# Performance work log

Hardware: AMD Instinct MI355X
Metric: run time of the kernel (lower is better)

Reference implementation:

```python
import jax, jax.numpy as jnp
import numpy as np

N_E = 8192
E_DIM = 64
BETA = 0.25
N_TOKENS = 32768


def setup_inputs() -> dict:
    key = jax.random.key(0)
    k1, k2 = jax.random.split(key)
    x = jax.random.normal(k1, (N_TOKENS, E_DIM), dtype=jnp.float32)
    # nn.Embedding weight initialized uniform(-1/n_e, 1/n_e)
    codebook = jax.random.uniform(k2, (N_E, E_DIM), dtype=jnp.float32,
                                  minval=-1.0 / N_E, maxval=1.0 / N_E)
    return {"x": x, "codebook": codebook, "start": 0, "end": N_E, "use_sk": 0}


def reference(x, codebook, start, end, use_sk):
    # use_sk=0 -> argmin branch (sinkhorn branch calls external helper, not exercised)
    latent = x.reshape(-1, E_DIM)                       # [N, D]
    cb = codebook[start:end]                            # [K, D]
    # squared euclidean distances: ||z||^2 + ||e||^2 - 2 z.e
    d = (jnp.sum(latent * latent, axis=1, keepdims=True)
         + jnp.sum(cb * cb, axis=1)[None, :]
         - 2.0 * jnp.einsum('nd,kd->nk', latent, cb))   # [N, K]
    indices = jnp.argmin(d, axis=-1) + start            # [N]
    x_q = codebook[indices].reshape(x.shape)            # gather
    sg = jax.lax.stop_gradient
    commitment_loss = jnp.mean((sg(x_q) - x) ** 2)
    codebook_loss = jnp.mean((x_q - sg(x)) ** 2)
    loss = codebook_loss + BETA * commitment_loss
    x_q_st = x + sg(x_q - x)                            # straight-through estimator
    indices = indices.reshape(x.shape[:-1])
    return x_q_st, loss, indices
```

## Files before the change

### kernel.cpp

```cpp
#include <hip/hip_runtime.h>
#include <math.h>


#define N_E    8192
#define EDIM   64
#define NTOK   32768
#define NELEM  (NTOK * EDIM)
#define CSZ    32
#define WINDOW 3e-4f
#define TTOK   128
#define TCODE  1024
#define SROW   72
#define TOKB   16
#define KCAP   256

typedef __attribute__((ext_vector_type(8)))  short          short8;
typedef __attribute__((ext_vector_type(8)))  unsigned short ushort8v;
typedef __attribute__((ext_vector_type(16))) float          f32x16;

__device__ __forceinline__ unsigned short f2bf(float f) {
  unsigned int u = __float_as_uint(f);
  return (unsigned short)((u + 0x7FFFu + ((u >> 16) & 1u)) >> 16);
}
__device__ __forceinline__ unsigned short f2h(float f) {
  union { _Float16 h; unsigned short u; } cv; cv.h = (_Float16)f; return cv.u;
}
__device__ __forceinline__ float h2f(unsigned short b) {
  union { _Float16 h; unsigned short u; } cv; cv.u = b; return (float)cv.h;
}
__device__ __forceinline__ float max16(const f32x16 a) {
  float m = fmaxf(fmaxf(a[0], a[1]), a[2]);
  m = fmaxf(fmaxf(m, a[3]),  a[4]);
  m = fmaxf(fmaxf(m, a[5]),  a[6]);
  m = fmaxf(fmaxf(m, a[7]),  a[8]);
  m = fmaxf(fmaxf(m, a[9]),  a[10]);
  m = fmaxf(fmaxf(m, a[11]), a[12]);
  m = fmaxf(fmaxf(m, a[13]), a[14]);
  return fmaxf(m, a[15]);
}
__device__ __forceinline__ float sx_of(const float4* xl4) {
#pragma clang fp contract(off)
  float a0=0,a1=0,a2=0,a3=0,a4=0,a5=0,a6=0,a7=0;
#pragma unroll
  for (int i = 0; i < 8; ++i) {
    float4 pA = xl4[2*i], pB = xl4[2*i+1];
    a0 += pA.x * pA.x; a1 += pA.y * pA.y; a2 += pA.z * pA.z; a3 += pA.w * pA.w;
    a4 += pB.x * pB.x; a5 += pB.y * pB.y; a6 += pB.z * pB.z; a7 += pB.w * pB.w;
  }
  return ((a0+a1) + (a2+a3)) + ((a4+a5) + (a6+a7));
}

__global__ __launch_bounds__(256) void vq_sc(const float* __restrict__ cb,
                                             float* __restrict__ sc,
                                             unsigned short* __restrict__ cbf) {
#pragma clang fp contract(off)
  int r = blockIdx.x * 256 + threadIdx.x;
  const float4* c4 = (const float4*)(cb + (size_t)r * EDIM);
  float sval = sx_of(c4);
  sc[r] = sval;
  unsigned short* dst = cbf + (size_t)r * EDIM;
#pragma unroll
  for (int h = 0; h < 8; ++h) {
    float4 fA = c4[2*h], fB = c4[2*h+1];
    ushort8v o = {f2bf(fA.x), f2bf(fA.y), f2bf(fA.z), f2bf(fA.w),
                  f2bf(fB.x), f2bf(fB.y), f2bf(fB.z), f2bf(fB.w)};
    *(ushort8v*)&dst[h * 8] = o;
  }
}

__global__ __launch_bounds__(256, 4) void vq_pass1(
    const float* __restrict__ x, const unsigned short* __restrict__ cbf,
    unsigned int* __restrict__ cand,
    const int* __restrict__ p_start, const int* __restrict__ p_end) {
  __shared__ unsigned short Cs[128 * SROW];
  __shared__ unsigned minL[128 * 17];
  int tid = threadIdx.x;
  int tb = blockIdx.x;
  int cbk = blockIdx.y;
  int s = *p_start, e = *p_end;
  const bool allfull = (cbk * TCODE >= s) && (cbk * TCODE + TCODE <= e);

  int lane = tid & 63, wv = tid >> 6;
  int half = lane >> 5, ln = lane & 31;
  int tokbase = wv * 32;

  const ushort8v* cg0 = (const ushort8v*)(cbf + (size_t)cbk * TCODE * EDIM);
#pragma unroll
  for (int p = 0; p < 4; ++p) {
    int idx = tid + p * 256;
    int row = idx >> 3, h = idx & 7;
    *(ushort8v*)&Cs[row * SROW + h * 8] = cg0[idx];
  }

  short8 bfr[4];
  {
    const float* xrow =
        x + (size_t)(tb * TTOK + tokbase + ln) * EDIM + half * 8;
#pragma unroll
    for (int ks = 0; ks < 4; ++ks) {
      float4 fA = *(const float4*)(xrow + ks * 16);
      float4 fB = *(const float4*)(xrow + ks * 16 + 4);
      short8 v = {(short)f2bf(fA.x), (short)f2bf(fA.y), (short)f2bf(fA.z),
                  (short)f2bf(fA.w), (short)f2bf(fB.x), (short)f2bf(fB.y),
                  (short)f2bf(fB.z), (short)f2bf(fB.w)};
      bfr[ks] = v;
    }
  }
  __syncthreads();

  unsigned short* minL16 = (unsigned short*)minL;

  for (int nb = 0; nb < 8; ++nb) {
    ushort8v creg[4];
    if (nb < 7) {
      const ushort8v* cg =
          (const ushort8v*)(cbf + ((size_t)cbk * TCODE + (nb + 1) * 128) * EDIM);
#pragma unroll
      for (int p = 0; p < 4; ++p) creg[p] = cg[tid + p * 256];
    }
#pragma unroll
    for (int cp = 0; cp < 2; ++cp) {
      f32x16 acc[2];
#pragma unroll
      for (int c2 = 0; c2 < 2; ++c2) acc[c2] = (f32x16)0.0f;
#pragma unroll
      for (int ks = 0; ks < 4; ++ks)
#pragma unroll
        for (int c2 = 0; c2 < 2; ++c2) {
          int ct = cp * 2 + c2;
          short8 a = *(const short8*)&Cs[(ct*32 + ln) * SROW + ks*16 + half*8];
          acc[c2] = __builtin_amdgcn_mfma_f32_32x32x16_bf16(a, bfr[ks],
                                                            acc[c2], 0, 0, 0);
        }
#pragma unroll
      for (int c2 = 0; c2 < 2; ++c2) {
        int cidL = nb * 4 + cp * 2 + c2;
        float v;
        if (allfull) {
          v = max16(acc[c2]);
        } else {
          int c0 = cbk * TCODE + cidL * 32;
          bool full = (c0 >= s) && (c0 + 32 <= e);
          if (full) {
            v = max16(acc[c2]);
          } else {
            v = -INFINITY;
#pragma unroll
            for (int r = 0; r < 16; ++r) {
              int code = c0 + (r & 3) + 8 * (r >> 2) + 4 * half;
              if (code >= s && code < e) v = fmaxf(v, acc[c2][r]);
            }
          }
        }
        v = fmaxf(v, __shfl_xor(v, 32, 64));
        if (!half)
          minL16[(tokbase + ln) * 34 + cidL] = f2h(-2.0f * v);
      }
    }
    __syncthreads();
    if (nb < 7) {
#pragma unroll
      for (int p = 0; p < 4; ++p) {
        int idx = tid + p * 256;
        int row = idx >> 3, h = idx & 7;
        *(ushort8v*)&Cs[row * SROW + h * 8] = creg[p];
      }
    }
    __syncthreads();
  }

#pragma unroll
  for (int p = 0; p < 2; ++p) {
    int idx = tid + p * 256;
    int tl = idx >> 2, part = idx & 3;
    const unsigned* src = minL + tl * 17 + part * 4;
    uint4 v; v.x = src[0]; v.y = src[1]; v.z = src[2]; v.w = src[3];
    *(uint4*)(cand + (((size_t)(tb * TTOK + tl)) * 8 + cbk) * 16 + part * 4) = v;
  }
}

__global__ __launch_bounds__(256) void vq_rescue(
    const float* __restrict__ x, const float* __restrict__ cb,
    const float* __restrict__ sc, const unsigned int* __restrict__ cand,
    float* __restrict__ out_xq, float* __restrict__ out_idx,
    float* __restrict__ partial,
    const int* __restrict__ p_start, const int* __restrict__ p_end) {
#pragma clang fp contract(off)
  __shared__ float xsh[TOKB][64];
  __shared__ float sxs[TOKB];
  __shared__ unsigned short clst[TOKB][KCAP];
  __shared__ int kcnt[TOKB];
  int tid  = threadIdx.x;
  int wv   = tid >> 6;
  int lane = tid & 63;
  int blk  = blockIdx.x;
  int s = *p_start, e = *p_end;

  if (tid < TOKB) kcnt[tid] = 0;
  __syncthreads();

  if (tid < 128) {
    int tl = tid >> 3, q = tid & 7;
    int gtok = blk * TOKB + tl;
    const uint4* rp = (const uint4*)(cand + ((size_t)gtok * 8 + q) * 16);
    uint4 A0 = rp[0], A1 = rp[1], A2 = rp[2], A3 = rp[3];
    unsigned rw[16] = {A0.x, A0.y, A0.z, A0.w, A1.x, A1.y, A1.z, A1.w,
                       A2.x, A2.y, A2.z, A2.w, A3.x, A3.y, A3.z, A3.w};
    float m = INFINITY;
#pragma unroll
    for (int j = 0; j < 16; ++j) {
      unsigned u = rw[j];
      m = fminf(m, fminf(h2f((unsigned short)(u & 0xFFFFu)),
                         h2f((unsigned short)(u >> 16))));
    }
    m = fminf(m, __shfl_xor(m, 1, 64));
    m = fminf(m, __shfl_xor(m, 2, 64));
    m = fminf(m, __shfl_xor(m, 4, 64));
    float thr = m + WINDOW;
#pragma unroll
    for (int j = 0; j < 16; ++j) {
      unsigned u = rw[j];
      if (h2f((unsigned short)(u & 0xFFFFu)) <= thr) {
        int i = atomicAdd(&kcnt[tl], 1);
        if (i < KCAP) clst[tl][i] = (unsigned short)(q * 32 + 2 * j);
      }
      if (h2f((unsigned short)(u >> 16)) <= thr) {
        int i = atomicAdd(&kcnt[tl], 1);
        if (i < KCAP) clst[tl][i] = (unsigned short)(q * 32 + 2 * j + 1);
      }
    }
  } else if (tid < 192) {
    int t = tid - 128;
#pragma unroll
    for (int p = 0; p < 4; ++p) {
      int idx = t + p * 64;
      int tl = idx >> 4, seg = idx & 15;
      *(float4*)&xsh[tl][seg * 4] =
          ((const float4*)(x + (size_t)(blk * TOKB + tl) * EDIM))[seg];
    }
  } else if (tid < 192 + TOKB) {
    int tl = tid - 192;
    sxs[tl] = sx_of((const float4*)(x + (size_t)(blk * TOKB + tl) * EDIM));
  }
  __syncthreads();

#define EVAL_CODE_BODY(K_, XL4) do {                                           \
    const float4* c4_ = (const float4*)(cb + (size_t)(K_) * EDIM);             \
    float t0_=0.0f,t1_=0.0f,t2_=0.0f,t3_=0.0f;                                 \
    _Pragma("unroll")                                                          \
    for (int i_ = 0; i_ < 8; ++i_) {                 \
      float4 v_ = c4_[2*i_ + h5_];                                             \
      float4 p_ = (XL4)[2*i_ + h5_];                                           \
      t0_ += v_.x * p_.x; t1_ += v_.y * p_.y;                                  \
      t2_ += v_.z * p_.z; t3_ += v_.w * p_.w;                                  \
    }                                                                          \
    s2_ = (t0_ + t1_) + (t2_ + t3_);              \
  } while (0)

#define FINISH_CODE(K_, ACT, SX, BP) do {                                      \
    float tt_ = s2_ + __shfl_xor(s2_, 1, 64);                                  \
    if ((ACT) && (K_) >= s && (K_) < e) {                                      \
      float d_ = ((SX) + sc[K_]) - 2.0f * tt_;                                 \
      unsigned db_ = __float_as_uint(d_);                                      \
      unsigned en_ = db_ ^ ((unsigned)((int)db_ >> 31) | 0x80000000u);         \
      unsigned long long pk_ = ((unsigned long long)en_ << 32) | (unsigned)(K_);\
      if (pk_ < (BP)) (BP) = pk_;                                              \
    }                                                                          \
  } while (0)

  float sg[4];
#pragma unroll
  for (int ti = 0; ti < 4; ++ti) {
    int tl = wv * 4 + ti;
    int gtok = blk * TOKB + tl;
    const float4* xl4 = (const float4*)xsh[tl];
    float sx = sxs[tl];
    unsigned long long bp = ~0ull;
    int ci_ = lane >> 1, h5_ = lane & 1;
    int nk = kcnt[tl]; if (nk > KCAP) nk = KCAP;
    for (int i = 0; i < nk; ++i) {
      int k_ = (int)clst[tl][i] * CSZ + ci_;
      float s2_;
      EVAL_CODE_BODY(k_, xl4);
      FINISH_CODE(k_, true, sx, bp);
    }
#pragma unroll
    for (int off = 32; off >= 1; off >>= 1) {
      unsigned long long o = __shfl_xor(bp, off, 64);
      if (o < bp) bp = o;
    }
    int bidx = (int)(unsigned)(bp & 0xFFFFFFFFull) & (N_E - 1);

    float xx = xsh[tl][lane];
    float qv = cb[(size_t)bidx * EDIM + lane];
    float diff = qv - xx;
    out_xq[(size_t)gtok * EDIM + lane] = xx + diff;
    if (lane == 0) out_idx[gtok] = (float)bidx;
    float l = diff * diff;
#pragma unroll
    for (int off = 32; off >= 1; off >>= 1) l += __shfl_down(l, off, 64);
    sg[ti] = l;
  }
#undef EVAL_CODE_BODY
#undef FINISH_CODE
  if (lane == 0)
    partial[blk * 4 + wv] = (sg[0] + sg[1]) + (sg[2] + sg[3]);
}

__global__ __launch_bounds__(256) void vq_loss(const float* __restrict__ partial,
                                               float* __restrict__ out_loss) {
  int tid = threadIdx.x;
  float s = 0.0f;
  for (int i = tid; i < NTOK / 4; i += 256) s += partial[i];
#pragma unroll
  for (int off = 32; off >= 1; off >>= 1) s += __shfl_down(s, off, 64);
  __shared__ float sdata[4];
  if ((tid & 63) == 0) sdata[tid >> 6] = s;
  __syncthreads();
  if (tid == 0) {
    float total = (sdata[0] + sdata[1]) + (sdata[2] + sdata[3]);
    float m = total * (1.0f / (float)NELEM);
    out_loss[0] = m + 0.25f * m;
  }
}

extern "C" void kernel_launch(void* const* d_in, const int* in_sizes, int n_in,
                              void* d_out, int out_size, void* d_ws, size_t ws_size,
                              hipStream_t stream) {
  const float* x  = (const float*)d_in[0];
  const float* cb = (const float*)d_in[1];
  const int* p_start = (const int*)d_in[2];
  const int* p_end   = (const int*)d_in[3];

  float* ws = (float*)d_ws;
  float* sc      = ws;
  float* partial = ws + N_E;
  unsigned short* cbf  = (unsigned short*)(ws + 2 * N_E);
  unsigned int*   cand = (unsigned int*)(cbf + (size_t)N_E * EDIM);

  float* out      = (float*)d_out;
  float* out_xq   = out;
  float* out_loss = out + NELEM;
  float* out_idx  = out + NELEM + 1;

  vq_sc<<<N_E / 256, 256, 0, stream>>>(cb, sc, cbf);
  dim3 g1(NTOK / TTOK, N_E / TCODE);
  vq_pass1<<<g1, 256, 0, stream>>>(x, cbf, cand, p_start, p_end);
  vq_rescue<<<NTOK / TOKB, 256, 0, stream>>>(x, cb, sc, cand, out_xq, out_idx,
                                             partial, p_start, p_end);
  vq_loss<<<1, 256, 0, stream>>>(partial, out_loss);
}
```

Before: 178.8 us.

## Balance rescue work with a shared block-wide job queue across waves

The rescue kernel used to give each wave four fixed tokens and walk each token's candidate chunk list serially, so waves whose tokens had many candidates held up the block. Candidates for all 16 tokens now go into one shared job list, and waves take two chunks at a time through an atomic counter. Each half-wave evaluates 32 codes with a full 64-wide dot product per lane instead of splitting it across lane pairs. The per-token minimum is then merged with a 64-bit atomicCAS in shared memory. This balances load and halves the chunk iterations, at the cost of atomic contention and shared-memory CAS loops.

Result: slower. 226.3 us (+26.6%).

```diff
diff --git a/kernel.cpp b/kernel.cpp
--- a/kernel.cpp
+++ b/kernel.cpp
@@ -12,7 +12,7 @@
 #define TCODE  1024
 #define SROW   72
 #define TOKB   16
-#define KCAP   256
+#define JCAP   4096
 
 typedef __attribute__((ext_vector_type(8)))  short          short8;
 typedef __attribute__((ext_vector_type(8)))  unsigned short ushort8v;
@@ -188,15 +188,17 @@
 #pragma clang fp contract(off)
   __shared__ float xsh[TOKB][64];
   __shared__ float sxs[TOKB];
-  __shared__ unsigned short clst[TOKB][KCAP];
-  __shared__ int kcnt[TOKB];
+  __shared__ unsigned short jobs[JCAP];
+  __shared__ unsigned long long bp[TOKB];
+  __shared__ int jcnt, jpos;
   int tid  = threadIdx.x;
   int wv   = tid >> 6;
   int lane = tid & 63;
   int blk  = blockIdx.x;
   int s = *p_start, e = *p_end;
 
-  if (tid < TOKB) kcnt[tid] = 0;
+  if (tid < TOKB) bp[tid] = ~0ull;
+  if (tid == 0) { jcnt = 0; jpos = 0; }
   __syncthreads();
 
   if (tid < 128) {
@@ -221,12 +223,12 @@
     for (int j = 0; j < 16; ++j) {
       unsigned u = rw[j];
       if (h2f((unsigned short)(u & 0xFFFFu)) <= thr) {
-        int i = atomicAdd(&kcnt[tl], 1);
-        if (i < KCAP) clst[tl][i] = (unsigned short)(q * 32 + 2 * j);
+        int i = atomicAdd(&jcnt, 1);
+        jobs[i] = (unsigned short)((tl << 8) | (q * 32 + 2 * j));
       }
       if (h2f((unsigned short)(u >> 16)) <= thr) {
-        int i = atomicAdd(&kcnt[tl], 1);
-        if (i < KCAP) clst[tl][i] = (unsigned short)(q * 32 + 2 * j + 1);
+        int i = atomicAdd(&jcnt, 1);
+        jobs[i] = (unsigned short)((tl << 8) | (q * 32 + 2 * j + 1));
       }
     }
   } else if (tid < 192) {
@@ -244,53 +246,63 @@
   }
   __syncthreads();
 
-#define EVAL_CODE_BODY(K_, XL4) do {                                           \
-    const float4* c4_ = (const float4*)(cb + (size_t)(K_) * EDIM);             \
-    float t0_=0.0f,t1_=0.0f,t2_=0.0f,t3_=0.0f;                                 \
-    _Pragma("unroll")                                                          \
-    for (int i_ = 0; i_ < 8; ++i_) {                 \
-      float4 v_ = c4_[2*i_ + h5_];                                             \
-      float4 p_ = (XL4)[2*i_ + h5_];                                           \
-      t0_ += v_.x * p_.x; t1_ += v_.y * p_.y;                                  \
-      t2_ += v_.z * p_.z; t3_ += v_.w * p_.w;                                  \
-    }                                                                          \
-    s2_ = (t0_ + t1_) + (t2_ + t3_);              \
-  } while (0)
-
-#define FINISH_CODE(K_, ACT, SX, BP) do {                                      \
-    float tt_ = s2_ + __shfl_xor(s2_, 1, 64);                                  \
-    if ((ACT) && (K_) >= s && (K_) < e) {                                      \
-      float d_ = ((SX) + sc[K_]) - 2.0f * tt_;                                 \
-      unsigned db_ = __float_as_uint(d_);                                      \
-      unsigned en_ = db_ ^ ((unsigned)((int)db_ >> 31) | 0x80000000u);         \
-      unsigned long long pk_ = ((unsigned long long)en_ << 32) | (unsigned)(K_);\
-      if (pk_ < (BP)) (BP) = pk_;                                              \
-    }                                                                          \
-  } while (0)
+  int n = jcnt;
+  int ln32 = lane & 31, half32 = lane >> 5;
+  for (;;) {
+    int idx = 0;
+    if (lane == 0) idx = atomicAdd(&jpos, 2);
+    idx = __shfl(idx, 0, 64);
+    if (idx >= n) break;
+    unsigned jA = jobs[idx];
+    bool haveB = (idx + 1 < n);
+    unsigned jB = haveB ? jobs[idx + 1] : jA;
+    unsigned jv = half32 ? jB : jA;
+    bool act = half32 ? haveB : true;
+    int tlh = (int)(jv >> 8) & 15;
+    int ch  = (int)(jv & 255u);
+    int k   = ch * CSZ + ln32;
+    const float4* c4 = (const float4*)(cb + (size_t)k * EDIM);
+    const float4* xl4 = (const float4*)xsh[tlh];
+    float sck = sc[k];
+    float sxh = sxs[tlh];
+    float t0=0,t1=0,t2=0,t3=0,t4=0,t5=0,t6=0,t7=0;
+#pragma unroll
+    for (int i = 0; i < 8; ++i) {
+      float4 cA = c4[2*i], cB = c4[2*i+1];
+      float4 pA = xl4[2*i], pB = xl4[2*i+1];
+      t0 += cA.x * pA.x; t1 += cA.y * pA.y; t2 += cA.z * pA.z; t3 += cA.w * pA.w;
+      t4 += cB.x * pB.x; t5 += cB.y * pB.y; t6 += cB.z * pB.z; t7 += cB.w * pB.w;
+    }
+    float tt = ((t0+t1) + (t2+t3)) + ((t4+t5) + (t6+t7));
+    unsigned long long pk = ~0ull;
+    if (act && k >= s && k < e) {
+      float d = (sxh + sck) - 2.0f * tt;
+      unsigned db = __float_as_uint(d);
+      unsigned en = db ^ ((unsigned)((int)db >> 31) | 0x80000000u);
+      pk = ((unsigned long long)en << 32) | (unsigned)k;
+    }
+#pragma unroll
+    for (int off = 16; off >= 1; off >>= 1) {
+      unsigned long long o = __shfl_xor(pk, off, 64);
+      if (o < pk) pk = o;
+    }
+    if (ln32 == 0 && pk != ~0ull) {
+      unsigned long long cur = bp[tlh];
+      while (pk < cur) {
+        unsigned long long pr = atomicCAS(&bp[tlh], cur, pk);
+        if (pr == cur) break;
+        cur = pr;
+      }
+    }
+  }
+  __syncthreads();
 
   float sg[4];
 #pragma unroll
   for (int ti = 0; ti < 4; ++ti) {
     int tl = wv * 4 + ti;
     int gtok = blk * TOKB + tl;
-    const float4* xl4 = (const float4*)xsh[tl];
-    float sx = sxs[tl];
-    unsigned long long bp = ~0ull;
-    int ci_ = lane >> 1, h5_ = lane & 1;
-    int nk = kcnt[tl]; if (nk > KCAP) nk = KCAP;
-    for (int i = 0; i < nk; ++i) {
-      int k_ = (int)clst[tl][i] * CSZ + ci_;
-      float s2_;
-      EVAL_CODE_BODY(k_, xl4);
-      FINISH_CODE(k_, true, sx, bp);
-    }
-#pragma unroll
-    for (int off = 32; off >= 1; off >>= 1) {
-      unsigned long long o = __shfl_xor(bp, off, 64);
-      if (o < bp) bp = o;
-    }
-    int bidx = (int)(unsigned)(bp & 0xFFFFFFFFull) & (N_E - 1);
-
+    int bidx = (int)(unsigned)(bp[tl] & 0xFFFFFFFFull) & (N_E - 1);
     float xx = xsh[tl][lane];
     float qv = cb[(size_t)bidx * EDIM + lane];
     float diff = qv - xx;
@@ -301,8 +313,6 @@
     for (int off = 32; off >= 1; off >>= 1) l += __shfl_down(l, off, 64);
     sg[ti] = l;
   }
-#undef EVAL_CODE_BODY
-#undef FINISH_CODE
   if (lane == 0)
     partial[blk * 4 + wv] = (sg[0] + sg[1]) + (sg[2] + sg[3]);
 }
```
